# Performance work log

Measured on AMD Instinct MI355X. Metric: run time of the kernel, lower is better.

## Reference

```python
import jax, jax.numpy as jnp
import numpy as np

NQ = 12          # n_qubits
DEPTH = 8        # vqc_depth
NCLASS = 10      # n_class
BATCH = 4096
DIM = 2 ** NQ    # statevector dimension


def _ry(theta):
    # RY(theta) = [[cos(t/2), -sin(t/2)], [sin(t/2), cos(t/2)]] (real)
    c = jnp.cos(theta / 2)
    s = jnp.sin(theta / 2)
    return jnp.stack([jnp.stack([c, -s], -1), jnp.stack([s, c], -1)], -2)


def _apply_1q(state, U, q):
    # state: [B, DIM] real; wire 0 = most-significant bit (PennyLane convention)
    B = state.shape[0]
    L = 2 ** q
    R = DIM // (2 * L)
    s = state.reshape(B, L, 2, R)
    if U.ndim == 2:   # shared gate
        s = jnp.einsum('ij,bljr->blir', U, s)
    else:             # per-sample gate [B,2,2]
        s = jnp.einsum('bij,bljr->blir', U, s)
    return s.reshape(B, DIM)


def _cnot_adj(state, i):
    # CNOT with control=i, target=i+1 (adjacent wires)
    B = state.shape[0]
    L = 2 ** i
    R = DIM // (4 * L)
    s = state.reshape(B, L, 2, 2, R)
    # control=0 block unchanged; control=1 block has target amplitudes swapped
    s = jnp.concatenate([s[:, :, :1], s[:, :, 1:, ::-1]], axis=2)
    return s.reshape(B, DIM)


def _vqc(X, weights):
    B = X.shape[0]
    # H on every wire applied to |0...0> gives the uniform positive state
    state = jnp.full((B, DIM), 2.0 ** (-NQ / 2), dtype=X.dtype)
    # data-encoding RY layer (per-sample angles)
    for q in range(NQ):
        state = _apply_1q(state, _ry(X[:, q]), q)
    # variational layers
    for k in range(DEPTH):
        for i in range(0, NQ - 1, 2):
            state = _cnot_adj(state, i)
        for i in range(1, NQ - 1, 2):
            state = _cnot_adj(state, i)
        for q in range(NQ):
            state = _apply_1q(state, _ry(weights[k, q]), q)
    # <Z_p> = P(bit p = 0) - P(bit p = 1); amplitudes are real
    probs = state * state  # [B, DIM]
    outs = []
    for p in range(NCLASS):
        L = 2 ** p
        R = DIM // (2 * L)
        pr = probs.reshape(B, L, 2, R)
        outs.append((pr[:, :, 0] - pr[:, :, 1]).sum(axis=(1, 2)))
    return jnp.stack(outs, axis=1)  # [B, NCLASS]


def setup_inputs() -> dict:
    key = jax.random.key(0)
    kx, kw = jax.random.split(key)
    X = jax.random.normal(kx, (BATCH, NQ), dtype=jnp.float32)
    weights = 0.01 * jax.random.normal(kw, (DEPTH, NQ), dtype=jnp.float32)
    return {"X": X, "weights": weights}


def reference(X, weights):
    return _vqc(X, weights)
```

## Files before the change

kernel.cpp:

```cpp
#include <hip/hip_runtime.h>
#include <hip/hip_fp16.h>

#define NQ 12
#define DEPTH 8
#define NCLASS 10
#define BATCH 4096
#define LSTRIDE 68
#define WPB 2


__device__ __forceinline__ uint32_t h2u(__half2 x) { return __builtin_bit_cast(uint32_t, x); }
__device__ __forceinline__ __half2 u2h(uint32_t x) { return __builtin_bit_cast(__half2, x); }

__device__ constexpr int hfun(int r) {
    const int rb5 = (r >> 5) & 1, rb4 = (r >> 4) & 1, rb3 = (r >> 3) & 1;
    const int rb2 = (r >> 2) & 1, rb1 = (r >> 1) & 1, rb0 = r & 1;
    const int c0 = rb5;
    const int c1 = rb4 ^ rb5;
    const int c2 = rb3 ^ rb4;
    const int c3 = rb2 ^ rb3 ^ rb4;
    const int c4 = rb1 ^ rb2;
    const int c5 = rb0 ^ rb1 ^ rb2;
    return (c0 << 5) | (c1 << 4) | (c2 << 3) | (c3 << 2) | (c4 << 1) | c5;
}

__device__ __forceinline__ void spair(uint32_t& a_, uint32_t& b_, __half2 Tp, __half2 Tn) {
    const __half2 a = u2h(a_), b = u2h(b_);
    a_ = h2u(__hfma2(Tn, b, a));
    b_ = h2u(__hfma2(Tp, a, b));
}

template <int M>
__device__ __forceinline__ void shearv(uint32_t (&v)[64], __half2 Tp, __half2 Tn) {
#pragma unroll
    for (int r = 0; r < 64; ++r) {
        if (r & M) continue;
        spair(v[r], v[r | M], Tp, Tn);
    }
}

__global__ __launch_bounds__(WPB * 64) void vqc_kernel(const float* __restrict__ X,
                                                       const float* __restrict__ W,
                                                       float* __restrict__ out) {
    __shared__ __align__(16) uint32_t lds[WPB * 64 * LSTRIDE];

    const int lane = threadIdx.x & 63;
    const int wid  = threadIdx.x >> 6;
    const int gw   = blockIdx.x * WPB + wid;
    const int s0   = 2 * gw, s1 = s0 + 1;
    const int l    = lane;

    uint32_t* Wb   = &lds[wid * 64 * LSTRIDE];
    uint32_t* wrow = &Wb[l * LSTRIDE];
    const int G = l ^ (l >> 1) ^ ((l >> 2) & 5);
    const uint32_t* colA = &Wb[G];
    const uint32_t* colB = &Wb[G ^ 0x30];
    const uint32_t* rT2  = &Wb[l];

    float cx0[NQ], sx0[NQ], cx1[NQ], sx1[NQ];
#pragma unroll
    for (int q = 0; q < NQ; ++q) {
        __sincosf(0.5f * X[s0 * NQ + q] + 0.78539816339744831f, &sx0[q], &cx0[q]);
        __sincosf(0.5f * X[s1 * NQ + q] + 0.78539816339744831f, &sx1[q], &cx1[q]);
    }
    float P0 = 1.0f, P1 = 1.0f;
#pragma unroll
    for (int q = 0; q < 6; ++q) {
        P0 *= ((l >> (5 - q)) & 1) ? sx0[q] : cx0[q];
        P1 *= ((l >> (5 - q)) & 1) ? sx1[q] : cx1[q];
    }

    uint32_t v[64];
    v[0] = h2u(__floats2half2_rn(P0 * cx0[11], P1 * cx1[11]));
    v[1] = h2u(__floats2half2_rn(P0 * sx0[11], P1 * sx1[11]));
#pragma unroll
    for (int lvl = 1; lvl < 6; ++lvl) {
        const int q = 11 - lvl;
        const __half2 SX = __floats2half2_rn(sx0[q], sx1[q]);
        const __half2 CX = __floats2half2_rn(cx0[q], cx1[q]);
#pragma unroll
        for (int j = 0; j < (1 << 5); ++j) {
            if (j >= (1 << lvl)) continue;
            v[j + (1 << lvl)] = h2u(__hmul2(u2h(v[j]), SX));
            v[j]              = h2u(__hmul2(u2h(v[j]), CX));
        }
    }

    float Call = 1.0f;

#pragma unroll 1
    for (int k = 0; k < DEPTH; ++k) {
        __half2 Tp[NQ], Tn[NQ];
#pragma unroll
        for (int q = 0; q < NQ; ++q) {
            float cw, sw;
            __sincosf(0.5f * W[k * NQ + q], &sw, &cw);
            Call *= cw;
            const float t = sw / cw;
            Tp[q] = __floats2half2_rn(t, t);
            Tn[q] = __floats2half2_rn(-t, -t);
        }

#pragma unroll
        for (int t = 0; t < 16; ++t)
            *(uint4*)&wrow[4 * t] = make_uint4(v[4 * t], v[4 * t + 1], v[4 * t + 2], v[4 * t + 3]);

#pragma unroll
        for (int m = 0; m < 32; ++m) {
            const int r  = ((m >> 1) << 2) | (m & 1);
            const int ha = hfun(r);
            const int hb = ha ^ 3;
            const int h0 = (ha < hb) ? ha : hb;
            const uint32_t* base = ((r & 1) ? colB : colA) + h0 * LSTRIDE;
            v[r]     = base[(ha - h0) * LSTRIDE];
            v[r | 2] = base[(hb - h0) * LSTRIDE];
        }

        shearv<32>(v, Tp[0], Tn[0]);
        shearv<16>(v, Tp[1], Tn[1]);
        shearv<8>(v, Tp[2], Tn[2]);
        shearv<4>(v, Tp[3], Tn[3]);
        shearv<2>(v, Tp[4], Tn[4]);
        shearv<1>(v, Tp[5], Tn[5]);

#pragma unroll
        for (int t = 0; t < 16; ++t)
            *(uint4*)&wrow[4 * t] = make_uint4(v[4 * t], v[4 * t + 1], v[4 * t + 2], v[4 * t + 3]);

#pragma unroll
        for (int m = 0; m < 32; ++m) {
            const uint32_t* base = rT2 + (2 * m) * LSTRIDE;
            v[2 * m]     = base[0];
            v[2 * m + 1] = base[LSTRIDE];
        }

        shearv<32>(v, Tp[6], Tn[6]);
        shearv<16>(v, Tp[7], Tn[7]);
        shearv<8>(v, Tp[8], Tn[8]);
        shearv<4>(v, Tp[9], Tn[9]);
        shearv<2>(v, Tp[10], Tn[10]);
        shearv<1>(v, Tp[11], Tn[11]);
    }

    const float C2 = (Call * Call);

    float c20[16], c21[16];
#pragma unroll
    for (int m = 0; m < 16; ++m) {
        float a0 = 0.0f, a1 = 0.0f;
#pragma unroll
        for (int i = 0; i < 4; ++i) {
            const float2 f = __half22float2(u2h(v[4 * m + i]));
            a0 += f.x * f.x;
            a1 += f.y * f.y;
        }
        c20[m] = a0;
        c21[m] = a1;
    }

    float S0 = 0.0f, S1 = 0.0f;
#pragma unroll
    for (int m = 0; m < 16; ++m) { S0 += c20[m]; S1 += c21[m]; }
    S0 *= C2; S1 *= C2;

    float T0[4], T1[4];
#pragma unroll
    for (int t = 0; t < 4; ++t) {
        float a0 = 0.0f, a1 = 0.0f;
#pragma unroll
        for (int m = 0; m < 16; ++m) {
            const float sgn = ((m >> t) & 1) ? -1.0f : 1.0f;
            a0 += sgn * c20[m];
            a1 += sgn * c21[m];
        }
        T0[t] = a0 * C2;
        T1[t] = a1 * C2;
    }

    float o0[NCLASS], o1[NCLASS];
#pragma unroll
    for (int p = 0; p < 6; ++p) {
        const float sgn = ((l >> (5 - p)) & 1) ? -1.0f : 1.0f;
        float r0 = sgn * S0, r1 = sgn * S1;
#pragma unroll
        for (int m = 0; m < 6; ++m) { r0 += __shfl_xor(r0, 1 << m, 64); r1 += __shfl_xor(r1, 1 << m, 64); }
        o0[p] = r0; o1[p] = r1;
    }
#pragma unroll
    for (int p = 6; p < 10; ++p) {
        float r0 = T0[9 - p], r1 = T1[9 - p];
#pragma unroll
        for (int m = 0; m < 6; ++m) { r0 += __shfl_xor(r0, 1 << m, 64); r1 += __shfl_xor(r1, 1 << m, 64); }
        o0[p] = r0; o1[p] = r1;
    }

    if (lane == 0) {
#pragma unroll
        for (int p = 0; p < NCLASS; ++p) {
            out[s0 * NCLASS + p] = o0[p];
            out[s1 * NCLASS + p] = o1[p];
        }
    }
}

extern "C" void kernel_launch(void* const* d_in, const int* in_sizes, int n_in,
                              void* d_out, int out_size, void* d_ws, size_t ws_size,
                              hipStream_t stream) {
    const float* X = (const float*)d_in[0];
    const float* W = (const float*)d_in[1];
    float* out     = (float*)d_out;
    (void)in_sizes; (void)n_in; (void)out_size; (void)d_ws; (void)ws_size;

    dim3 grid(BATCH / (2 * WPB));
    dim3 block(WPB * 64);
    hipLaunchKernelGGL(vqc_kernel, grid, block, 0, stream, X, W, out);
}
```

Before: 97.18 us.

## Split each sample pair's statevector across two waves with cross-half lane exchange

Each sample pair is now handled by two wavefronts in one block instead of one wavefront. Each lane holds 32 amplitudes instead of 64, and the LDS transpose is shared between the waves, separated by block barriers. The gate on the qubit spread across the two 32-lane halves is applied with a permlane32 swap, or a shuffle as fallback, plus an FMA. This halves register pressure to raise occupancy and parallelism, at the cost of added __syncthreads, lane exchanges and a final cross-wave reduction through LDS.

```diff
diff --git a/kernel.cpp b/kernel.cpp
--- a/kernel.cpp
+++ b/kernel.cpp
@@ -6,8 +6,9 @@
 #define NCLASS 10
 #define BATCH 4096
 #define LSTRIDE 68
-#define WPB 2
-
+
+
+typedef unsigned int uint2v __attribute__((ext_vector_type(2)));
 
 __device__ __forceinline__ uint32_t h2u(__half2 x) { return __builtin_bit_cast(uint32_t, x); }
 __device__ __forceinline__ __half2 u2h(uint32_t x) { return __builtin_bit_cast(__half2, x); }
@@ -24,38 +25,55 @@
     return (c0 << 5) | (c1 << 4) | (c2 << 3) | (c3 << 2) | (c4 << 1) | c5;
 }
 
-__device__ __forceinline__ void spair(uint32_t& a_, uint32_t& b_, __half2 Tp, __half2 Tn) {
+__device__ __forceinline__ uint32_t xchg32(uint32_t x, int lane) {
+#if __has_builtin(__builtin_amdgcn_permlane32_swap)
+    uint2v pr = __builtin_amdgcn_permlane32_swap(x, x, false, false);
+    return (lane < 32) ? pr.y : pr.x;
+#else
+    return (uint32_t)__shfl_xor((int)x, 32, 64);
+#endif
+}
+
+__device__ __forceinline__ void spair(uint32_t& a_, uint32_t& b_, __half2 T) {
     const __half2 a = u2h(a_), b = u2h(b_);
-    a_ = h2u(__hfma2(Tn, b, a));
-    b_ = h2u(__hfma2(Tp, a, b));
+    a_ = h2u(__hfma2(__hneg2(T), b, a));
+    b_ = h2u(__hfma2(T, a, b));
 }
 
 template <int M>
-__device__ __forceinline__ void shearv(uint32_t (&v)[64], __half2 Tp, __half2 Tn) {
-#pragma unroll
-    for (int r = 0; r < 64; ++r) {
+__device__ __forceinline__ void shear_reg(uint32_t (&v)[32], __half2 T) {
+#pragma unroll
+    for (int r = 0; r < 32; ++r) {
         if (r & M) continue;
-        spair(v[r], v[r | M], Tp, Tn);
-    }
-}
-
-__global__ __launch_bounds__(WPB * 64) void vqc_kernel(const float* __restrict__ X,
-                                                       const float* __restrict__ W,
-                                                       float* __restrict__ out) {
-    __shared__ __align__(16) uint32_t lds[WPB * 64 * LSTRIDE];
-
-    const int lane = threadIdx.x & 63;
-    const int wid  = threadIdx.x >> 6;
-    const int gw   = blockIdx.x * WPB + wid;
-    const int s0   = 2 * gw, s1 = s0 + 1;
-    const int l    = lane;
-
-    uint32_t* Wb   = &lds[wid * 64 * LSTRIDE];
-    uint32_t* wrow = &Wb[l * LSTRIDE];
+        spair(v[r], v[r | M], T);
+    }
+}
+
+__device__ __forceinline__ float wave_sum(float r) {
+#pragma unroll
+    for (int m = 0; m < 6; ++m) r += __shfl_xor(r, 1 << m, 64);
+    return r;
+}
+
+__global__ __launch_bounds__(128) void vqc_kernel(const float* __restrict__ X,
+                                                  const float* __restrict__ W,
+                                                  float* __restrict__ out) {
+    __shared__ __align__(16) uint32_t lds[64 * LSTRIDE];
+    __shared__ float red[2][2][NCLASS];
+
+    const int l  = threadIdx.x & 63;
+    const int w  = threadIdx.x >> 6;
+    const int s0 = 2 * blockIdx.x, s1 = s0 + 1;
+
+    uint32_t* wptr = &lds[l * LSTRIDE + 32 * w];
     const int G = l ^ (l >> 1) ^ ((l >> 2) & 5);
-    const uint32_t* colA = &Wb[G];
-    const uint32_t* colB = &Wb[G ^ 0x30];
-    const uint32_t* rT2  = &Wb[l];
+    const int ro0 = w ? 48 * LSTRIDE : 0;
+    const int ro1 = w ? 16 * LSTRIDE : 0;
+    const uint32_t* r1_00 = &lds[G + ro0];
+    const uint32_t* r1_10 = &lds[(G ^ 0x30) + ro0];
+    const uint32_t* r1_01 = &lds[G + ro1];
+    const uint32_t* r1_11 = &lds[(G ^ 0x30) + ro1];
+    const uint32_t* r2    = &lds[(32 * w) * LSTRIDE + l];
 
     float cx0[NQ], sx0[NQ], cx1[NQ], sx1[NQ];
 #pragma unroll
@@ -63,23 +81,24 @@
         __sincosf(0.5f * X[s0 * NQ + q] + 0.78539816339744831f, &sx0[q], &cx0[q]);
         __sincosf(0.5f * X[s1 * NQ + q] + 0.78539816339744831f, &sx1[q], &cx1[q]);
     }
-    float P0 = 1.0f, P1 = 1.0f;
+    float P0 = w ? sx0[6] : cx0[6];
+    float P1 = w ? sx1[6] : cx1[6];
 #pragma unroll
     for (int q = 0; q < 6; ++q) {
         P0 *= ((l >> (5 - q)) & 1) ? sx0[q] : cx0[q];
         P1 *= ((l >> (5 - q)) & 1) ? sx1[q] : cx1[q];
     }
 
-    uint32_t v[64];
+    uint32_t v[32];
     v[0] = h2u(__floats2half2_rn(P0 * cx0[11], P1 * cx1[11]));
     v[1] = h2u(__floats2half2_rn(P0 * sx0[11], P1 * sx1[11]));
 #pragma unroll
-    for (int lvl = 1; lvl < 6; ++lvl) {
+    for (int lvl = 1; lvl < 5; ++lvl) {
         const int q = 11 - lvl;
         const __half2 SX = __floats2half2_rn(sx0[q], sx1[q]);
         const __half2 CX = __floats2half2_rn(cx0[q], cx1[q]);
 #pragma unroll
-        for (int j = 0; j < (1 << 5); ++j) {
+        for (int j = 0; j < 16; ++j) {
             if (j >= (1 << lvl)) continue;
             v[j + (1 << lvl)] = h2u(__hmul2(u2h(v[j]), SX));
             v[j]              = h2u(__hmul2(u2h(v[j]), CX));
@@ -90,63 +109,75 @@
 
 #pragma unroll 1
     for (int k = 0; k < DEPTH; ++k) {
-        __half2 Tp[NQ], Tn[NQ];
+        __half2 T[NQ];
 #pragma unroll
         for (int q = 0; q < NQ; ++q) {
             float cw, sw;
             __sincosf(0.5f * W[k * NQ + q], &sw, &cw);
             Call *= cw;
             const float t = sw / cw;
-            Tp[q] = __floats2half2_rn(t, t);
-            Tn[q] = __floats2half2_rn(-t, -t);
-        }
-
-#pragma unroll
-        for (int t = 0; t < 16; ++t)
-            *(uint4*)&wrow[4 * t] = make_uint4(v[4 * t], v[4 * t + 1], v[4 * t + 2], v[4 * t + 3]);
-
-#pragma unroll
-        for (int m = 0; m < 32; ++m) {
-            const int r  = ((m >> 1) << 2) | (m & 1);
-            const int ha = hfun(r);
-            const int hb = ha ^ 3;
-            const int h0 = (ha < hb) ? ha : hb;
-            const uint32_t* base = ((r & 1) ? colB : colA) + h0 * LSTRIDE;
-            v[r]     = base[(ha - h0) * LSTRIDE];
-            v[r | 2] = base[(hb - h0) * LSTRIDE];
-        }
-
-        shearv<32>(v, Tp[0], Tn[0]);
-        shearv<16>(v, Tp[1], Tn[1]);
-        shearv<8>(v, Tp[2], Tn[2]);
-        shearv<4>(v, Tp[3], Tn[3]);
-        shearv<2>(v, Tp[4], Tn[4]);
-        shearv<1>(v, Tp[5], Tn[5]);
-
-#pragma unroll
-        for (int t = 0; t < 16; ++t)
-            *(uint4*)&wrow[4 * t] = make_uint4(v[4 * t], v[4 * t + 1], v[4 * t + 2], v[4 * t + 3]);
-
-#pragma unroll
-        for (int m = 0; m < 32; ++m) {
-            const uint32_t* base = rT2 + (2 * m) * LSTRIDE;
-            v[2 * m]     = base[0];
-            v[2 * m + 1] = base[LSTRIDE];
-        }
-
-        shearv<32>(v, Tp[6], Tn[6]);
-        shearv<16>(v, Tp[7], Tn[7]);
-        shearv<8>(v, Tp[8], Tn[8]);
-        shearv<4>(v, Tp[9], Tn[9]);
-        shearv<2>(v, Tp[10], Tn[10]);
-        shearv<1>(v, Tp[11], Tn[11]);
-    }
-
-    const float C2 = (Call * Call);
-
-    float c20[16], c21[16];
-#pragma unroll
-    for (int m = 0; m < 16; ++m) {
+            T[q] = __floats2half2_rn(t, t);
+        }
+
+#pragma unroll
+        for (int t8 = 0; t8 < 8; ++t8)
+            *(uint4*)&wptr[4 * t8] = make_uint4(v[4 * t8], v[4 * t8 + 1],
+                                                v[4 * t8 + 2], v[4 * t8 + 3]);
+        __syncthreads();
+
+#pragma unroll
+        for (int j = 0; j < 32; ++j) {
+            const uint32_t* base = (j & 16) ? ((j & 1) ? r1_11 : r1_01)
+                                            : ((j & 1) ? r1_10 : r1_00);
+            v[j] = base[hfun(j) * LSTRIDE];
+        }
+
+        shear_reg<16>(v, T[1]);
+        shear_reg<8>(v, T[2]);
+        shear_reg<4>(v, T[3]);
+        shear_reg<2>(v, T[4]);
+        shear_reg<1>(v, T[5]);
+        {
+            const __half2 tS = (l < 32) ? __hneg2(T[6]) : T[6];
+#pragma unroll
+            for (int j = 0; j < 32; ++j) {
+                const uint32_t p = xchg32(v[j], l);
+                v[j] = h2u(__hfma2(tS, u2h(p), u2h(v[j])));
+            }
+        }
+        __syncthreads();
+
+#pragma unroll
+        for (int t8 = 0; t8 < 8; ++t8)
+            *(uint4*)&wptr[4 * t8] = make_uint4(v[4 * t8], v[4 * t8 + 1],
+                                                v[4 * t8 + 2], v[4 * t8 + 3]);
+        __syncthreads();
+
+#pragma unroll
+        for (int j = 0; j < 32; ++j)
+            v[j] = r2[j * LSTRIDE];
+
+        shear_reg<16>(v, T[7]);
+        shear_reg<8>(v, T[8]);
+        shear_reg<4>(v, T[9]);
+        shear_reg<2>(v, T[10]);
+        shear_reg<1>(v, T[11]);
+        {
+            const __half2 tS = (l < 32) ? __hneg2(T[0]) : T[0];
+#pragma unroll
+            for (int j = 0; j < 32; ++j) {
+                const uint32_t p = xchg32(v[j], l);
+                v[j] = h2u(__hfma2(tS, u2h(p), u2h(v[j])));
+            }
+        }
+        __syncthreads();
+    }
+
+    const float C2 = Call * Call;
+
+    float c20[8], c21[8];
+#pragma unroll
+    for (int m = 0; m < 8; ++m) {
         float a0 = 0.0f, a1 = 0.0f;
 #pragma unroll
         for (int i = 0; i < 4; ++i) {
@@ -160,15 +191,15 @@
 
     float S0 = 0.0f, S1 = 0.0f;
 #pragma unroll
-    for (int m = 0; m < 16; ++m) { S0 += c20[m]; S1 += c21[m]; }
+    for (int m = 0; m < 8; ++m) { S0 += c20[m]; S1 += c21[m]; }
     S0 *= C2; S1 *= C2;
 
-    float T0[4], T1[4];
-#pragma unroll
-    for (int t = 0; t < 4; ++t) {
+    float T0[3], T1[3];
+#pragma unroll
+    for (int t = 0; t < 3; ++t) {
         float a0 = 0.0f, a1 = 0.0f;
 #pragma unroll
-        for (int m = 0; m < 16; ++m) {
+        for (int m = 0; m < 8; ++m) {
             const float sgn = ((m >> t) & 1) ? -1.0f : 1.0f;
             a0 += sgn * c20[m];
             a1 += sgn * c21[m];
@@ -177,29 +208,35 @@
         T1[t] = a1 * C2;
     }
 
-    float o0[NCLASS], o1[NCLASS];
+    float p0[NCLASS], p1[NCLASS];
 #pragma unroll
     for (int p = 0; p < 6; ++p) {
         const float sgn = ((l >> (5 - p)) & 1) ? -1.0f : 1.0f;
-        float r0 = sgn * S0, r1 = sgn * S1;
-#pragma unroll
-        for (int m = 0; m < 6; ++m) { r0 += __shfl_xor(r0, 1 << m, 64); r1 += __shfl_xor(r1, 1 << m, 64); }
-        o0[p] = r0; o1[p] = r1;
-    }
-#pragma unroll
-    for (int p = 6; p < 10; ++p) {
-        float r0 = T0[9 - p], r1 = T1[9 - p];
-#pragma unroll
-        for (int m = 0; m < 6; ++m) { r0 += __shfl_xor(r0, 1 << m, 64); r1 += __shfl_xor(r1, 1 << m, 64); }
-        o0[p] = r0; o1[p] = r1;
-    }
-
-    if (lane == 0) {
+        p0[p] = wave_sum(sgn * S0);
+        p1[p] = wave_sum(sgn * S1);
+    }
+    {
+        const float ws = w ? -1.0f : 1.0f;
+        p0[6] = ws * wave_sum(S0);
+        p1[6] = ws * wave_sum(S1);
+    }
+#pragma unroll
+    for (int p = 7; p < 10; ++p) {
+        p0[p] = wave_sum(T0[9 - p]);
+        p1[p] = wave_sum(T1[9 - p]);
+    }
+
+    if (l == 0) {
 #pragma unroll
         for (int p = 0; p < NCLASS; ++p) {
-            out[s0 * NCLASS + p] = o0[p];
-            out[s1 * NCLASS + p] = o1[p];
-        }
+            red[w][0][p] = p0[p];
+            red[w][1][p] = p1[p];
+        }
+    }
+    __syncthreads();
+    if (threadIdx.x < 2 * NCLASS) {
+        const int s = threadIdx.x / NCLASS, p = threadIdx.x % NCLASS;
+        out[(s0 + s) * NCLASS + p] = red[0][s][p] + red[1][s][p];
     }
 }
 
@@ -211,7 +248,7 @@
     float* out     = (float*)d_out;
     (void)in_sizes; (void)n_in; (void)out_size; (void)d_ws; (void)ws_size;
 
-    dim3 grid(BATCH / (2 * WPB));
-    dim3 block(WPB * 64);
+    dim3 grid(BATCH / 2);
+    dim3 block(128);
     hipLaunchKernelGGL(vqc_kernel, grid, block, 0, stream, X, W, out);
 }
```

After: 118.8 us. 1.22x slower.
